# Kernel optimization log

Hardware: AMD Instinct MI355X
Metric: run time of the kernel (lower is better)

## Reference

```python
import jax, jax.numpy as jnp
import numpy as np
from jax import lax

B, CIN, HID, T, H, W = 4, 32, 32, 31, 96, 96


def setup_inputs() -> dict:
    key = jax.random.key(0)
    k1, k2, k3 = jax.random.split(key, 3)
    inputs = jax.random.normal(k1, (B, CIN, T, H, W), dtype=jnp.float32)
    conv_w = jax.random.normal(k2, (2 * HID, CIN, 3, 3, 3), dtype=jnp.float32) * 0.05
    conv_b = jax.random.normal(k3, (2 * HID,), dtype=jnp.float32) * 0.05
    gamma = jnp.ones((1,), dtype=jnp.float32)
    return {"inputs": inputs, "conv_w": conv_w, "conv_b": conv_b, "gamma": gamma}


def reference(inputs, conv_w, conv_b, gamma):
    hid = conv_w.shape[0] // 2
    # Conv3d, 'same' padding, NCDHW layout -> gates [B, 2*hid, T, H, W]
    gates = lax.conv_general_dilated(
        inputs, conv_w, window_strides=(1, 1, 1), padding="SAME",
        dimension_numbers=("NCDHW", "OIDHW", "NCDHW"))
    gates = gates + conv_b[None, :, None, None, None]
    Z = jnp.tanh(gates[:, :hid])          # [B, hid, T, H, W]
    F = jax.nn.sigmoid(gates[:, hid:])    # [B, hid, T, H, W]

    # Gated recurrence over time (dim 2): h_t = f_t * h_{t-1} + (1 - f_t) * z_t
    Zt = jnp.moveaxis(Z, 2, 0)  # [T, B, hid, H, W]
    Ft = jnp.moveaxis(F, 2, 0)

    def step(h, zf):
        z, f = zf
        h = f * h + (1.0 - f) * z
        return h, h

    h0 = jnp.zeros_like(Zt[0])  # h=None <=> h0=0 since f*0+(1-f)*z
    _, hs = lax.scan(step, h0, (Zt, Ft))
    h_time = jnp.moveaxis(hs, 0, 2)  # [B, hid, T, H, W]

    # Per-spatial-location channel attention
    qh = jnp.transpose(h_time, (0, 3, 4, 1, 2))  # [B, H, W, C, T]
    scores = jnp.einsum("bhwct,bhwdt->bhwcd", qh, qh)  # [B, H, W, C, C]
    attn = jax.nn.softmax(scores, axis=3)  # softmax over row axis c (dim=3), as in torch
    attn = attn * (1.0 / np.sqrt(qh.shape[-2]))  # divide AFTER softmax by sqrt(C)
    ah = jnp.einsum("bhwcd,bhwdt->bhwct", attn, qh)  # [B, H, W, C, T]
    ah = jnp.transpose(ah, (0, 3, 4, 1, 2))  # [B, C, T, H, W]

    return gamma * ah + h_time
```

## Files before the change

kernel.cpp:

```cpp
#include <hip/hip_runtime.h>
#include <math.h>

#define B_ 4
#define CIN_ 32
#define HID_ 32
#define T_ 31
#define H_ 96
#define W_ 96
#define SP_ (H_*W_)
#define TSP (T_ * SP_)

typedef _Float16 half8 __attribute__((ext_vector_type(8)));
typedef float f32x4 __attribute__((ext_vector_type(4)));
typedef float f32x16 __attribute__((ext_vector_type(16)));

static __device__ inline unsigned int packhh(float a, float b) {
  unsigned short ua = __builtin_bit_cast(unsigned short, (_Float16)a);
  unsigned short ub = __builtin_bit_cast(unsigned short, (_Float16)b);
  return (unsigned int)ua | ((unsigned int)ub << 16);
}

__global__ __launch_bounds__(256) void prep_w_kernel(
    const float* __restrict__ w, _Float16* __restrict__ wr) {
  int idx = blockIdx.x * 256 + threadIdx.x;
  if (idx >= 55296) return;
  int i = idx & 7;
  int lane = (idx >> 3) & 63;
  int rest = idx >> 9;
  int tap = rest % 27;
  int ocg = rest / 27;
  int m = lane & 15;
  int cin = (lane >> 4) * 8 + i;
  int oc = (m & 1) * 32 + ocg * 8 + (m >> 1);
  wr[idx] = (_Float16)(w[(oc * CIN_ + cin) * 27 + tap]);
}

#define PITCH 40
#define SROWS 8
#define SCOLS 18
#define RST (SCOLS * PITCH)
#define SLICE_HF (SROWS * RST)

__global__ __launch_bounds__(256, 2) void conv_rec_mfma(
    const float* __restrict__ in, const _Float16* __restrict__ wr,
    const float* __restrict__ bias, unsigned int* __restrict__ gout) {
  __shared__ _Float16 in_s[4 * SLICE_HF];

  const int tid = threadIdx.x;
  const int tile = blockIdx.x;
  const int b = blockIdx.y;
  const int x0 = (tile % 6) * 16;
  const int y0 = (tile / 6) * 6;
  const int lane = tid & 63;
  const int ocg = tid >> 6;
  const int px = lane & 15;
  const int kq = lane >> 4;

  half8 wreg[27];
  {
    const _Float16* wp = wr + (size_t)ocg * 27 * 512 + lane * 8;
#pragma unroll
    for (int tap = 0; tap < 27; ++tap)
      wreg[tap] = *(const half8*)(wp + tap * 512);
  }

  const int c0 = ocg * 8 + 2 * kq;
  f32x4 bias4;
  bias4[0] = bias[c0];
  bias4[1] = bias[32 + c0];
  bias4[2] = bias[c0 + 1];
  bias4[3] = bias[32 + c0 + 1];

  const int s_xi = tid & 15;
  const int s_q  = tid >> 4;
  const int ibase = s_q * TSP + (y0 - 1) * W_ + x0 + s_xi;
  const int wxm   = ((s_xi + 1) & 8) ? 1 : 0;
  const int wbase = (s_xi + 1) * PITCH + s_q;
  const int e_cin = tid & 31;
  const int e_yy  = tid >> 5;
  const int e_gy  = y0 - 1 + e_yy;
  const bool e_ok = ((unsigned)e_gy < (unsigned)H_);
  const int eoff  = e_cin * TSP + e_gy * W_;
  const int ew0   = e_yy * RST + 0 * PITCH + e_cin;
  const int ew1   = e_yy * RST + 17 * PITCH + e_cin;
  const bool has_l = (x0 > 0), has_r = (x0 + 16 < W_);

  int cs[3];
#pragma unroll
  for (int kw = 0; kw < 3; ++kw) {
    int c = px + kw;
    cs[kw] = c * PITCH + ((kq * 8) ^ ((c & 8) ? 16 : 0));
  }

  const float* inb = in + (size_t)(b * CIN_) * TSP;

  auto stage_full = [&](int ts) {
    _Float16* dst = in_s + (ts & 3) * SLICE_HF;
    const int tso = ts * SP_;
#pragma unroll
    for (int k = 0; k < 16; ++k) {
      const int gy = y0 - 1 + (k >> 1);
      float v = 0.f;
      if ((unsigned)gy < (unsigned)H_)
        v = inb[ibase + (k & 1) * 16 * TSP + (k >> 1) * W_ + tso];
      dst[wbase + (k >> 1) * RST + (((k & 1) ^ wxm) * 16)] = (_Float16)v;
    }
    float v0 = 0.f, v1 = 0.f;
    if (e_ok) {
      if (has_l) v0 = inb[eoff + tso + x0 - 1];
      if (has_r) v1 = inb[eoff + tso + x0 + 16];
    }
    dst[ew0] = (_Float16)v0;
    dst[ew1] = (_Float16)v1;
  };

  {
    uint32_t* dz = (uint32_t*)(in_s + 3 * SLICE_HF);
    for (int e = tid; e < SLICE_HF / 2; e += 256) dz[e] = 0u;
  }
  stage_full(0);
  stage_full(1);
  __syncthreads();

  float h[6][2];
#pragma unroll
  for (int r = 0; r < 6; ++r) { h[r][0] = 0.f; h[r][1] = 0.f; }

  const int pr = ocg * 4 + kq;
  size_t obase = ((size_t)(b * 32 + pr) * T_) * SP_ + y0 * W_ + x0 + px;

  for (int t = 0; t < T_; ++t) {
    const int ts = t + 2;

    float sv[16], ev0 = 0.f, ev1 = 0.f;
    if (ts < T_) {
      const int tso = ts * SP_;
#pragma unroll
      for (int k = 0; k < 16; ++k) {
        const int gy = y0 - 1 + (k >> 1);
        sv[k] = 0.f;
        if ((unsigned)gy < (unsigned)H_)
          sv[k] = inb[ibase + (k & 1) * 16 * TSP + (k >> 1) * W_ + tso];
      }
      if (e_ok) {
        if (has_l) ev0 = inb[eoff + tso + x0 - 1];
        if (has_r) ev1 = inb[eoff + tso + x0 + 16];
      }
    }

    f32x4 acc[6];
#pragma unroll
    for (int r = 0; r < 6; ++r) acc[r] = bias4;

#pragma unroll
    for (int kd = 0; kd < 3; ++kd) {
      const _Float16* sb2 = in_s + ((t + 3 + kd) & 3) * SLICE_HF;
#pragma unroll
      for (int kw = 0; kw < 3; ++kw) {
        half8 brow[8];
#pragma unroll
        for (int rr = 0; rr < 8; ++rr)
          brow[rr] = *(const half8*)(sb2 + rr * RST + cs[kw]);
#pragma unroll
        for (int kh = 0; kh < 3; ++kh) {
          const int tap = kd * 9 + kh * 3 + kw;
#pragma unroll
          for (int r = 0; r < 6; ++r)
            acc[r] = __builtin_amdgcn_mfma_f32_16x16x32_f16(wreg[tap], brow[r + kh], acc[r], 0, 0, 0);
        }
      }
    }

    if (ts < T_) {
      _Float16* dst = in_s + (ts & 3) * SLICE_HF;
#pragma unroll
      for (int k = 0; k < 16; ++k)
        dst[wbase + (k >> 1) * RST + (((k & 1) ^ wxm) * 16)] = (_Float16)sv[k];
      dst[ew0] = (_Float16)ev0;
      dst[ew1] = (_Float16)ev1;
    } else if (ts == T_) {
      uint32_t* dz = (uint32_t*)(in_s + (ts & 3) * SLICE_HF);
      for (int e = tid; e < SLICE_HF / 2; e += 256) dz[e] = 0u;
    }

    unsigned int pk[6];
#pragma unroll
    for (int r = 0; r < 6; ++r) {
      float z0 = 1.f - 2.f / (1.f + __expf(2.f * acc[r][0]));
      float f0 = 1.f / (1.f + __expf(-acc[r][1]));
      h[r][0] = f0 * h[r][0] + (1.f - f0) * z0;
      float z1 = 1.f - 2.f / (1.f + __expf(2.f * acc[r][2]));
      float f1 = 1.f / (1.f + __expf(-acc[r][3]));
      h[r][1] = f1 * h[r][1] + (1.f - f1) * z1;
      pk[r] = packhh(h[r][0], h[r][1]);
    }
    __syncthreads();

#pragma unroll
    for (int r = 0; r < 6; ++r)
      gout[obase + r * W_] = pk[r];
    obase += SP_;
  }
}

#define APIT 40
#define PSTR 1288

__global__ __launch_bounds__(512) void attn_mfma(
    unsigned int* __restrict__ g, const float* __restrict__ gamma) {
  __shared__ _Float16 qh_s[16 * PSTR];
  __shared__ _Float16 qt_s[16 * PSTR];
  __shared__ _Float16 at_s[8 * 32 * APIT];

  const int tid = threadIdx.x;
  const int x0 = blockIdx.x * 16;
  const int y = blockIdx.y;
  const int b = blockIdx.z;
  const int lane = tid & 63;
  const int wv = tid >> 6;
  const float gm = gamma[0];

  for (int e = tid; e < 16 * 16 * 31; e += 512) {
    int xi = e & 15;
    int q = e >> 4;
    int t = q % 31;
    int pr = q / 31;
    unsigned int gw = g[((size_t)(b * 32 + pr) * T_ + t) * SP_ + y * W_ + x0 + xi];
    _Float16 h0 = __builtin_bit_cast(_Float16, (unsigned short)(gw & 0xffff));
    _Float16 h1 = __builtin_bit_cast(_Float16, (unsigned short)(gw >> 16));
    int c0 = 2 * pr;
    qh_s[xi * PSTR + c0 * APIT + t] = h0;
    qh_s[xi * PSTR + (c0 + 1) * APIT + t] = h1;
    qt_s[xi * PSTR + t * APIT + c0] = h0;
    qt_s[xi * PSTR + t * APIT + c0 + 1] = h1;
  }
  qh_s[(tid & 15) * PSTR + (tid >> 4) * APIT + 31] = (_Float16)0.f;
  __syncthreads();

  const int cd = lane & 31;
  const int hi = lane >> 5;

#pragma unroll
  for (int pp = 0; pp < 2; ++pp) {
    const int px = wv * 2 + pp;
    const _Float16* qs = qh_s + px * PSTR;
    const _Float16* qt = qt_s + px * PSTR;
    _Float16* as = at_s + wv * (32 * APIT);

    half8 q0 = *(const half8*)(qs + cd * APIT + hi * 8);
    half8 q1 = *(const half8*)(qs + cd * APIT + hi * 8 + 16);
    f32x16 S = {};
    S = __builtin_amdgcn_mfma_f32_32x32x16_f16(q0, q0, S, 0, 0, 0);
    S = __builtin_amdgcn_mfma_f32_32x32x16_f16(q1, q1, S, 0, 0, 0);

    float mx = S[0];
#pragma unroll
    for (int r = 1; r < 16; ++r) mx = fmaxf(mx, S[r]);
    mx = fmaxf(mx, __shfl_xor(mx, 32));
    float sm = 0.f;
    float ev[16];
#pragma unroll
    for (int r = 0; r < 16; ++r) { ev[r] = __expf(S[r] - mx); sm += ev[r]; }
    sm += __shfl_xor(sm, 32);
    const float sc = 0.17677669529663688f / sm;

#pragma unroll
    for (int r = 0; r < 16; ++r) {
      int c = (r & 3) + 8 * (r >> 2) + 4 * hi;
      as[c * APIT + cd] = (_Float16)(ev[r] * sc);
    }

    half8 a0 = *(const half8*)(as + cd * APIT + hi * 8);
    half8 a1 = *(const half8*)(as + cd * APIT + hi * 8 + 16);
    half8 b0 = *(const half8*)(qt + cd * APIT + hi * 8);
    half8 b1 = *(const half8*)(qt + cd * APIT + hi * 8 + 16);
    f32x16 P = {};
    P = __builtin_amdgcn_mfma_f32_32x32x16_f16(a0, b0, P, 0, 0, 0);
    P = __builtin_amdgcn_mfma_f32_32x32x16_f16(a1, b1, P, 0, 0, 0);

#pragma unroll
    for (int r = 0; r < 16; ++r) {
      int c = (r & 3) + 8 * (r >> 2) + 4 * hi;
      qt_s[px * PSTR + cd * APIT + c] = (_Float16)P[r];
    }
  }
  __syncthreads();

  float* gf = (float*)g;
  for (int e = tid; e < 4 * 992; e += 512) {
    int xi4 = e & 3;
    int q = e >> 2;
    int t = q % 31;
    int c = q / 31;
    float4 rv;
#pragma unroll
    for (int j = 0; j < 4; ++j) {
      int xi = xi4 * 4 + j;
      float ah = (float)qt_s[xi * PSTR + t * APIT + c];
      float hv = (float)qh_s[xi * PSTR + c * APIT + t];
      (&rv.x)[j] = gm * ah + hv;
    }
    *(float4*)&gf[((size_t)(b * HID_ + c) * T_ + t) * SP_ + y * W_ + x0 +
                  xi4 * 4] = rv;
  }
}

extern "C" void kernel_launch(void* const* d_in, const int* in_sizes, int n_in,
                              void* d_out, int out_size, void* d_ws,
                              size_t ws_size, hipStream_t stream) {
  const float* in    = (const float*)d_in[0];
  const float* w     = (const float*)d_in[1];
  const float* bias  = (const float*)d_in[2];
  const float* gamma = (const float*)d_in[3];
  _Float16* wr = (_Float16*)d_ws;

  prep_w_kernel<<<216, 256, 0, stream>>>(w, wr);
  conv_rec_mfma<<<dim3(96, 4), 256, 0, stream>>>(
      in, wr, bias, (unsigned int*)d_out);
  attn_mfma<<<dim3(6, 96, 4), 512, 0, stream>>>(
      (unsigned int*)d_out, gamma);
}
```

Measured before the change: 277.8 us.

## Deepen conv input prefetch to two slices ahead with six-slot LDS ring

The conv+recurrence kernel now issues global loads for time slice t+3 while computing slice t, using two alternating register buffers and a 6-slot shared-memory ring instead of 4 slots. The goal is to hide more global-load latency behind the MFMA work. Occupancy is lowered to 1 block per SM via launch bounds to make room for the extra registers and LDS. The LDS layout also drops the XOR swizzle and uses a new cin-major staging mapping, which risks bank conflicts, and the recurrence update is rewritten into FMA form.

```diff
diff --git a/kernel.cpp b/kernel.cpp
--- a/kernel.cpp
+++ b/kernel.cpp
@@ -40,11 +40,96 @@
 #define SCOLS 18
 #define RST (SCOLS * PITCH)
 #define SLICE_HF (SROWS * RST)
-
-__global__ __launch_bounds__(256, 2) void conv_rec_mfma(
+#define SLOT(s) ((((s) % 6) + 6) % 6)
+
+#define ISSUE_LOADS(ts, sv, ev0, ev1)                                   \
+  {                                                                     \
+    const int tso = (ts) * SP_;                                         \
+    _Pragma("unroll")                                                   \
+    for (int k = 0; k < 16; ++k) {                                      \
+      int rj = k * 16 + s_q;                                            \
+      int cin = rj & 31;                                                \
+      int yy = rj >> 5;                                                 \
+      int gy = y0 - 1 + yy;                                             \
+      sv[k] = 0.f;                                                      \
+      if ((unsigned)gy < (unsigned)H_)                                  \
+        sv[k] = inb[(size_t)cin * TSP + tso + gy * W_ + x0 + s_xi];     \
+    }                                                                   \
+    ev0 = 0.f; ev1 = 0.f;                                               \
+    if (e_ok) {                                                         \
+      const float* rb = inb + (size_t)e_cin * TSP + tso + e_gy * W_;    \
+      if (has_l) ev0 = rb[x0 - 1];                                      \
+      if (has_r) ev1 = rb[x0 + 16];                                     \
+    }                                                                   \
+  }
+
+#define WRITE_SLICE(ts, sv, ev0, ev1)                                   \
+  {                                                                     \
+    _Float16* dst = in_s + SLOT(ts) * SLICE_HF;                         \
+    _Pragma("unroll")                                                   \
+    for (int k = 0; k < 16; ++k) {                                      \
+      int rj = k * 16 + s_q;                                            \
+      int cin = rj & 31;                                                \
+      int yy = rj >> 5;                                                 \
+      dst[(yy * SCOLS + s_xi + 1) * PITCH + cin] = (_Float16)sv[k];     \
+    }                                                                   \
+    dst[(e_yy * SCOLS + 0) * PITCH + e_cin] = (_Float16)ev0;            \
+    dst[(e_yy * SCOLS + 17) * PITCH + e_cin] = (_Float16)ev1;           \
+  }
+
+#define PHASE(tcur, svW, evW0, evW1, svL, evL0, evL1)                   \
+  {                                                                     \
+    const int tsL = (tcur) + 3;                                         \
+    if (tsL < T_) ISSUE_LOADS(tsL, svL, evL0, evL1);                    \
+    f32x4 acc[6];                                                       \
+    _Pragma("unroll") for (int r = 0; r < 6; ++r) acc[r] = bias4;       \
+    _Pragma("unroll")                                                   \
+    for (int kd = 0; kd < 3; ++kd) {                                    \
+      const _Float16* sb2 = in_s + SLOT((tcur) - 1 + kd) * SLICE_HF;    \
+      _Pragma("unroll")                                                 \
+      for (int kw = 0; kw < 3; ++kw) {                                  \
+        half8 brow[8];                                                  \
+        _Pragma("unroll")                                               \
+        for (int rr = 0; rr < 8; ++rr)                                  \
+          brow[rr] = *(const half8*)(sb2 + rr * RST + cs[kw]);          \
+        _Pragma("unroll")                                               \
+        for (int kh = 0; kh < 3; ++kh) {                                \
+          const int tap = kd * 9 + kh * 3 + kw;                         \
+          _Pragma("unroll")                                             \
+          for (int r = 0; r < 6; ++r)                                   \
+            acc[r] = __builtin_amdgcn_mfma_f32_16x16x32_f16(            \
+                wreg[tap], brow[r + kh], acc[r], 0, 0, 0);              \
+        }                                                               \
+      }                                                                 \
+    }                                                                   \
+    const int tsW = (tcur) + 2;                                         \
+    if (tsW < T_) {                                                     \
+      WRITE_SLICE(tsW, svW, evW0, evW1);                                \
+    } else if (tsW == T_) {                                             \
+      uint32_t* dz = (uint32_t*)(in_s + SLOT(T_) * SLICE_HF);           \
+      for (int e = tid; e < SLICE_HF / 2; e += 256) dz[e] = 0u;         \
+    }                                                                   \
+    unsigned int pk[6];                                                 \
+    _Pragma("unroll")                                                   \
+    for (int r = 0; r < 6; ++r) {                                       \
+      float z0 = 1.f - 2.f / (1.f + __expf(2.f * acc[r][0]));           \
+      float f0 = 1.f / (1.f + __expf(-acc[r][1]));                      \
+      h[r][0] = f0 * (h[r][0] - z0) + z0;                               \
+      float z1 = 1.f - 2.f / (1.f + __expf(2.f * acc[r][2]));           \
+      float f1 = 1.f / (1.f + __expf(-acc[r][3]));                      \
+      h[r][1] = f1 * (h[r][1] - z1) + z1;                               \
+      pk[r] = packhh(h[r][0], h[r][1]);                                 \
+    }                                                                   \
+    __syncthreads();                                                    \
+    _Pragma("unroll")                                                   \
+    for (int r = 0; r < 6; ++r) gout[obase + r * W_] = pk[r];           \
+    obase += SP_;                                                       \
+  }
+
+__global__ __launch_bounds__(256, 1) void conv_rec_mfma(
     const float* __restrict__ in, const _Float16* __restrict__ wr,
     const float* __restrict__ bias, unsigned int* __restrict__ gout) {
-  __shared__ _Float16 in_s[4 * SLICE_HF];
+  __shared__ _Float16 in_s[6 * SLICE_HF];
 
   const int tid = threadIdx.x;
   const int tile = blockIdx.x;
@@ -73,53 +158,29 @@
 
   const int s_xi = tid & 15;
   const int s_q  = tid >> 4;
-  const int ibase = s_q * TSP + (y0 - 1) * W_ + x0 + s_xi;
-  const int wxm   = ((s_xi + 1) & 8) ? 1 : 0;
-  const int wbase = (s_xi + 1) * PITCH + s_q;
   const int e_cin = tid & 31;
   const int e_yy  = tid >> 5;
   const int e_gy  = y0 - 1 + e_yy;
   const bool e_ok = ((unsigned)e_gy < (unsigned)H_);
-  const int eoff  = e_cin * TSP + e_gy * W_;
-  const int ew0   = e_yy * RST + 0 * PITCH + e_cin;
-  const int ew1   = e_yy * RST + 17 * PITCH + e_cin;
   const bool has_l = (x0 > 0), has_r = (x0 + 16 < W_);
 
+  const float* inb = in + (size_t)(b * CIN_) * TSP;
+
   int cs[3];
 #pragma unroll
-  for (int kw = 0; kw < 3; ++kw) {
-    int c = px + kw;
-    cs[kw] = c * PITCH + ((kq * 8) ^ ((c & 8) ? 16 : 0));
-  }
-
-  const float* inb = in + (size_t)(b * CIN_) * TSP;
-
-  auto stage_full = [&](int ts) {
-    _Float16* dst = in_s + (ts & 3) * SLICE_HF;
-    const int tso = ts * SP_;
-#pragma unroll
-    for (int k = 0; k < 16; ++k) {
-      const int gy = y0 - 1 + (k >> 1);
-      float v = 0.f;
-      if ((unsigned)gy < (unsigned)H_)
-        v = inb[ibase + (k & 1) * 16 * TSP + (k >> 1) * W_ + tso];
-      dst[wbase + (k >> 1) * RST + (((k & 1) ^ wxm) * 16)] = (_Float16)v;
-    }
-    float v0 = 0.f, v1 = 0.f;
-    if (e_ok) {
-      if (has_l) v0 = inb[eoff + tso + x0 - 1];
-      if (has_r) v1 = inb[eoff + tso + x0 + 16];
-    }
-    dst[ew0] = (_Float16)v0;
-    dst[ew1] = (_Float16)v1;
-  };
+  for (int kw = 0; kw < 3; ++kw) cs[kw] = (px + kw) * PITCH + kq * 8;
 
   {
-    uint32_t* dz = (uint32_t*)(in_s + 3 * SLICE_HF);
+    uint32_t* dz = (uint32_t*)(in_s + 5 * SLICE_HF);
     for (int e = tid; e < SLICE_HF / 2; e += 256) dz[e] = 0u;
   }
-  stage_full(0);
-  stage_full(1);
+  float svA[16], evA0 = 0.f, evA1 = 0.f;
+  float svB[16], evB0 = 0.f, evB1 = 0.f;
+  ISSUE_LOADS(0, svA, evA0, evA1);
+  WRITE_SLICE(0, svA, evA0, evA1);
+  ISSUE_LOADS(1, svA, evA0, evA1);
+  WRITE_SLICE(1, svA, evA0, evA1);
+  ISSUE_LOADS(2, svB, evB0, evB1);
   __syncthreads();
 
   float h[6][2];
@@ -129,78 +190,11 @@
   const int pr = ocg * 4 + kq;
   size_t obase = ((size_t)(b * 32 + pr) * T_) * SP_ + y0 * W_ + x0 + px;
 
-  for (int t = 0; t < T_; ++t) {
-    const int ts = t + 2;
-
-    float sv[16], ev0 = 0.f, ev1 = 0.f;
-    if (ts < T_) {
-      const int tso = ts * SP_;
-#pragma unroll
-      for (int k = 0; k < 16; ++k) {
-        const int gy = y0 - 1 + (k >> 1);
-        sv[k] = 0.f;
-        if ((unsigned)gy < (unsigned)H_)
-          sv[k] = inb[ibase + (k & 1) * 16 * TSP + (k >> 1) * W_ + tso];
-      }
-      if (e_ok) {
-        if (has_l) ev0 = inb[eoff + tso + x0 - 1];
-        if (has_r) ev1 = inb[eoff + tso + x0 + 16];
-      }
-    }
-
-    f32x4 acc[6];
-#pragma unroll
-    for (int r = 0; r < 6; ++r) acc[r] = bias4;
-
-#pragma unroll
-    for (int kd = 0; kd < 3; ++kd) {
-      const _Float16* sb2 = in_s + ((t + 3 + kd) & 3) * SLICE_HF;
-#pragma unroll
-      for (int kw = 0; kw < 3; ++kw) {
-        half8 brow[8];
-#pragma unroll
-        for (int rr = 0; rr < 8; ++rr)
-          brow[rr] = *(const half8*)(sb2 + rr * RST + cs[kw]);
-#pragma unroll
-        for (int kh = 0; kh < 3; ++kh) {
-          const int tap = kd * 9 + kh * 3 + kw;
-#pragma unroll
-          for (int r = 0; r < 6; ++r)
-            acc[r] = __builtin_amdgcn_mfma_f32_16x16x32_f16(wreg[tap], brow[r + kh], acc[r], 0, 0, 0);
-        }
-      }
-    }
-
-    if (ts < T_) {
-      _Float16* dst = in_s + (ts & 3) * SLICE_HF;
-#pragma unroll
-      for (int k = 0; k < 16; ++k)
-        dst[wbase + (k >> 1) * RST + (((k & 1) ^ wxm) * 16)] = (_Float16)sv[k];
-      dst[ew0] = (_Float16)ev0;
-      dst[ew1] = (_Float16)ev1;
-    } else if (ts == T_) {
-      uint32_t* dz = (uint32_t*)(in_s + (ts & 3) * SLICE_HF);
-      for (int e = tid; e < SLICE_HF / 2; e += 256) dz[e] = 0u;
-    }
-
-    unsigned int pk[6];
-#pragma unroll
-    for (int r = 0; r < 6; ++r) {
-      float z0 = 1.f - 2.f / (1.f + __expf(2.f * acc[r][0]));
-      float f0 = 1.f / (1.f + __expf(-acc[r][1]));
-      h[r][0] = f0 * h[r][0] + (1.f - f0) * z0;
-      float z1 = 1.f - 2.f / (1.f + __expf(2.f * acc[r][2]));
-      float f1 = 1.f / (1.f + __expf(-acc[r][3]));
-      h[r][1] = f1 * h[r][1] + (1.f - f1) * z1;
-      pk[r] = packhh(h[r][0], h[r][1]);
-    }
-    __syncthreads();
-
-#pragma unroll
-    for (int r = 0; r < 6; ++r)
-      gout[obase + r * W_] = pk[r];
-    obase += SP_;
-  }
+  for (int t0 = 0; t0 < T_ - 1; t0 += 2) {
+    PHASE(t0,     svB, evB0, evB1, svA, evA0, evA1);
+    PHASE(t0 + 1, svA, evA0, evA1, svB, evB0, evB1);
+  }
+  PHASE(T_ - 1, svB, evB0, evB1, svA, evA0, evA1);
 }
 
 #define APIT 40
```

Result: slower. 297.2 us (+7.0%).
